# Kernel optimization log

Hardware: AMD Instinct MI355X
Metric: run time of the kernel (lower is better)

## Reference

```python
import jax, jax.numpy as jnp
import numpy as np
import math

B = 8192
N_MODELS = 64
T_PER_SPLIT = 16
MAXLEAF = 64
EMB = 32
BN_EPS = 1e-5


def setup_inputs() -> dict:
    key = jax.random.key(0)
    k1, k2, k3 = jax.random.split(key, 3)
    # leaf indices per (sample, model*tree), values in [0, maxleaf)
    x = jax.random.randint(k1, (B, N_MODELS * T_PER_SPLIT), 0, MAXLEAF, dtype=jnp.int32)
    # embed_w ~ N(0, sqrt(1/max_ntree_per_split))
    embed_w = jax.random.normal(k2, (N_MODELS, T_PER_SPLIT * MAXLEAF, EMB), dtype=jnp.float32) * math.sqrt(1.0 / T_PER_SPLIT)
    # BatchNorm1d affine params (gamma=1, beta=0 at init)
    bn_gamma = jnp.ones((N_MODELS * EMB,), dtype=jnp.float32)
    bn_beta = jnp.zeros((N_MODELS * EMB,), dtype=jnp.float32)
    # BatchDense(n_models, embsize, 1): weight (M, E, 1) squeezed to (M, E), bias zeros (M,)
    stdv = math.sqrt(6.0 / (EMB + 1))
    bout_w = jax.random.uniform(k3, (N_MODELS, EMB), dtype=jnp.float32, minval=-stdv, maxval=stdv)
    bout_b = jnp.zeros((N_MODELS,), dtype=jnp.float32)
    return {"x": x, "embed_w": embed_w, "bn_gamma": bn_gamma, "bn_beta": bn_beta,
            "bout_w": bout_w, "bout_b": bout_b}


def reference(x, embed_w, bn_gamma, bn_beta, bout_w, bout_b):
    # x: (B, M*T) int leaf indices; embed_w: (M, T*L, E)
    Bn = x.shape[0]
    M, TL, E = embed_w.shape
    T = x.shape[1] // M
    L = TL // T
    # one_hot + bmm == per-tree gather from embed_w, summed over trees
    idx = x.reshape(Bn, M, T) + jnp.arange(T, dtype=x.dtype) * L  # (B, M, T) into TL axis
    emb = embed_w[jnp.arange(M)[None, :, None], idx]              # (B, M, T, E) gather
    h = emb.sum(axis=2).reshape(Bn, M * E)                        # (B, M*E)
    # BatchNorm1d (training-mode batch statistics, biased variance as in torch)
    mean = h.mean(axis=0)
    var = h.var(axis=0)
    h = (h - mean) / jnp.sqrt(var + BN_EPS) * bn_gamma + bn_beta
    # dropout is identity in eval mode
    h = h.reshape(Bn, M, E)
    # BatchDense: per-model linear E -> 1
    out = jnp.einsum('bme,me->bm', h, bout_w) + bout_b            # (B, M)
    sum_out = out.sum(axis=-1, keepdims=True)                     # (B, 1)
    return (sum_out, out)
```

## Files before the change

### kernel.cpp

```cpp
#include <hip/hip_runtime.h>
#include <hip/hip_fp16.h>

constexpr int B_TOT = 8192;
constexpr int NM    = 64;
constexpr int TT    = 16;
constexpr int LF    = 64;
constexpr int EM    = 32;
constexpr int XROW  = NM * TT;
constexpr int TROWS = TT * LF;

__global__ __launch_bounds__(512, 4) void k_stats_f16(
    const int* __restrict__ x, const float* __restrict__ tbl,
    float* __restrict__ wsum, float* __restrict__ wsumsq)
{
    __shared__ uint4 tb[TROWS * 4];
    __shared__ float red[2][8][32];

    const int m     = blockIdx.x & 63;
    const int chunk = blockIdx.x >> 6;
    const int tid   = threadIdx.x;
    const int f     = tid & 3;
    const int grp   = tid >> 2;
    const int b0    = chunk * 1024;

    {
        const float4* __restrict__ src = (const float4*)(tbl + (size_t)m * (TROWS * EM));
#pragma unroll
        for (int i = 0; i < 8; ++i) {
            const int o = tid + i * 512;
            const float4 a = src[o * 2];
            const float4 c = src[o * 2 + 1];
            uint4 p;
            __half2 h0 = __floats2half2_rn(a.x, a.y);
            __half2 h1 = __floats2half2_rn(a.z, a.w);
            __half2 h2 = __floats2half2_rn(c.x, c.y);
            __half2 h3 = __floats2half2_rn(c.z, c.w);
            p.x = *(unsigned*)&h0; p.y = *(unsigned*)&h1;
            p.z = *(unsigned*)&h2; p.w = *(unsigned*)&h3;
            tb[o] = p;
        }
    }

    const int4* xp = (const int4*)(x + (size_t)(b0 + grp) * XROW + m * TT);
    int4 xa = xp[0], xb_ = xp[1], xc = xp[2], xd = xp[3];

    float s[8], s2[8];
#pragma unroll
    for (int k = 0; k < 8; ++k) { s[k] = 0.f; s2[k] = 0.f; }

    __syncthreads();

    for (int p = 0; p < 8; ++p) {
        int4 na, nb, nc, nd;
        if (p < 7) {
            const int4* np = (const int4*)(x + (size_t)(b0 + (p + 1) * 128 + grp) * XROW + m * TT);
            na = np[0]; nb = np[1]; nc = np[2]; nd = np[3];
        }

        __half2 h[4];
#pragma unroll
        for (int k = 0; k < 4; ++k) h[k] = __half2(__half(0.f), __half(0.f));

#pragma unroll
        for (int tq = 0; tq < 4; ++tq) {
            const int4 q = (tq == 0) ? xa : (tq == 1) ? xb_ : (tq == 2) ? xc : xd;
            const int rbase = tq * 256;
            const uint4 v0 = tb[(q.x + rbase      ) * 4 + f];
            const uint4 v1 = tb[(q.y + rbase +  64) * 4 + f];
            const uint4 v2 = tb[(q.z + rbase + 128) * 4 + f];
            const uint4 v3 = tb[(q.w + rbase + 192) * 4 + f];
            h[0] = __hadd2(h[0], __hadd2(__hadd2(*(const __half2*)&v0.x, *(const __half2*)&v1.x),
                                         __hadd2(*(const __half2*)&v2.x, *(const __half2*)&v3.x)));
            h[1] = __hadd2(h[1], __hadd2(__hadd2(*(const __half2*)&v0.y, *(const __half2*)&v1.y),
                                         __hadd2(*(const __half2*)&v2.y, *(const __half2*)&v3.y)));
            h[2] = __hadd2(h[2], __hadd2(__hadd2(*(const __half2*)&v0.z, *(const __half2*)&v1.z),
                                         __hadd2(*(const __half2*)&v2.z, *(const __half2*)&v3.z)));
            h[3] = __hadd2(h[3], __hadd2(__hadd2(*(const __half2*)&v0.w, *(const __half2*)&v1.w),
                                         __hadd2(*(const __half2*)&v2.w, *(const __half2*)&v3.w)));
        }

#pragma unroll
        for (int k = 0; k < 4; ++k) {
            const float lo = __low2float(h[k]);
            const float hi = __high2float(h[k]);
            s[2*k]   += lo;  s2[2*k]   = fmaf(lo, lo, s2[2*k]);
            s[2*k+1] += hi;  s2[2*k+1] = fmaf(hi, hi, s2[2*k+1]);
        }

        xa = na; xb_ = nb; xc = nc; xd = nd;
    }

#pragma unroll
    for (int off = 4; off <= 32; off <<= 1) {
#pragma unroll
        for (int k = 0; k < 8; ++k) {
            s[k]  += __shfl_xor(s[k],  off);
            s2[k] += __shfl_xor(s2[k], off);
        }
    }
    const int wave = tid >> 6;
    if ((tid & 63) < 4) {
#pragma unroll
        for (int k = 0; k < 8; ++k) {
            red[0][wave][f * 8 + k] = s[k];
            red[1][wave][f * 8 + k] = s2[k];
        }
    }
    __syncthreads();
    if (tid < 32) {
        float a = 0.f, a2 = 0.f;
#pragma unroll
        for (int w = 0; w < 8; ++w) { a += red[0][w][tid]; a2 += red[1][w][tid]; }
        atomicAdd(&wsum[m * EM + tid], a);
        atomicAdd(&wsumsq[m * EM + tid], a2);
    }
}

__global__ __launch_bounds__(256) void k_prep(
    const float* __restrict__ tbl,
    const float* __restrict__ gamma, const float* __restrict__ beta,
    const float* __restrict__ bw, const float* __restrict__ bb,
    const float* __restrict__ wsum, const float* __restrict__ wsumsq,
    float* __restrict__ Cm, float* __restrict__ g2)
{
    const int m    = blockIdx.x >> 2;
    const int part = blockIdx.x & 3;
    __shared__ float a_s[EM];
    if (threadIdx.x < EM) {
        const int e  = threadIdx.x;
        const int ch = m * EM + e;
        const float inv_n = 1.f / (float)B_TOT;
        const float mean = wsum[ch] * inv_n;
        const float var  = wsumsq[ch] * inv_n - mean * mean;
        const float istd = rsqrtf(var + 1e-5f);
        const float g = gamma[ch];
        const float w = bw[ch];
        a_s[e] = istd * g * w;
        float ct = (beta[ch] - mean * istd * g) * w;
#pragma unroll
        for (int off = 16; off > 0; off >>= 1) ct += __shfl_down(ct, off, 32);
        if (e == 0 && part == 0) Cm[m] = bb[m] + ct;
    }
    __syncthreads();

    const float* __restrict__ tblm = tbl + (size_t)m * (TROWS * EM);
    const int row = part * 256 + threadIdx.x;
    const float4* rp = (const float4*)(tblm + row * EM);
    float acc = 0.f;
#pragma unroll
    for (int i = 0; i < 8; ++i) {
        const float4 v = rp[i];
        acc += v.x * a_s[i*4+0] + v.y * a_s[i*4+1]
             + v.z * a_s[i*4+2] + v.w * a_s[i*4+3];
    }
    g2[row * NM + m] = acc;
}

__global__ __launch_bounds__(1024, 8) void k_out(
    const int* __restrict__ x, const float* __restrict__ g2,
    const float* __restrict__ Cm, float* __restrict__ out)
{
    __shared__ float slab[4 * LF * NM];
    const int tid  = threadIdx.x;
    const int wid  = tid >> 6;
    const int lane = tid & 63;
    const int b    = blockIdx.x * 16 + wid;

    const int4* xp = (const int4*)(x + (size_t)b * XROW + lane * TT);
    const int4 q0 = xp[0], q1 = xp[1], q2 = xp[2], q3 = xp[3];
    const int idxs[16] = {q0.x,q0.y,q0.z,q0.w, q1.x,q1.y,q1.z,q1.w,
                          q2.x,q2.y,q2.z,q2.w, q3.x,q3.y,q3.z,q3.w};

    float acc = 0.f;
#pragma unroll
    for (int ph = 0; ph < 4; ++ph) {
        if (ph) __syncthreads();
        const float4* src = (const float4*)(g2 + (size_t)ph * (4 * LF * NM));
        float4* dst = (float4*)slab;
#pragma unroll
        for (int j = 0; j < 4; ++j) dst[tid + j * 1024] = src[tid + j * 1024];
        __syncthreads();
#pragma unroll
        for (int tt = 0; tt < 4; ++tt)
            acc += slab[tt * (LF * NM) + idxs[ph * 4 + tt] * NM + lane];
    }

    const float o = acc + Cm[lane];
    float s = o;
#pragma unroll
    for (int off = 32; off > 0; off >>= 1) s += __shfl_down(s, off);
    out[B_TOT + (size_t)b * NM + lane] = o;
    if (lane == 0) out[b] = s;
}

extern "C" void kernel_launch(void* const* d_in, const int* in_sizes, int n_in,
                              void* d_out, int out_size, void* d_ws, size_t ws_size,
                              hipStream_t stream) {
    const int*   x       = (const int*)d_in[0];
    const float* embed_w = (const float*)d_in[1];
    const float* gamma   = (const float*)d_in[2];
    const float* beta    = (const float*)d_in[3];
    const float* bout_w  = (const float*)d_in[4];
    const float* bout_b  = (const float*)d_in[5];
    float* out = (float*)d_out;

    float* ws     = (float*)d_ws;
    float* wsum   = ws;
    float* wsumsq = ws + 2048;
    float* Cm     = ws + 4096;
    float* g2     = ws + 4160;

    (void)hipMemsetAsync(wsum, 0, 4096 * sizeof(float), stream);

    k_stats_f16<<<dim3(512), dim3(512), 0, stream>>>(x, embed_w, wsum, wsumsq);
    k_prep<<<dim3(256), dim3(256),  0, stream>>>(embed_w, gamma, beta, bout_w,
                                                 bout_b, wsum, wsumsq, Cm, g2);
    k_out <<<dim3(512), dim3(1024), 0, stream>>>(x, g2, Cm, out);
}
```

Measured before the change: 111.4 us.

## Load x rows cooperatively with DPP broadcast and drop memset via per-chunk partials

In the stats kernel, each of the four lanes sharing a sample now loads only one int4 of that sample's leaf indices instead of all four, and DPP quad broadcasts share the values across the quad. This cuts redundant global loads and register pressure. The atomic accumulation into zeroed buffers is replaced by per-chunk partial sums that k_prep adds up, which removes the memset launch and the atomics. The cost is four extra DPP moves per gathered int4 and eight partial reads per channel in k_prep.

Result: faster. 108.0 us (-3.0%).

```diff
diff --git a/kernel.cpp b/kernel.cpp
--- a/kernel.cpp
+++ b/kernel.cpp
@@ -9,9 +9,22 @@
 constexpr int XROW  = NM * TT;
 constexpr int TROWS = TT * LF;
 
+template<int TQ>
+__device__ __forceinline__ int4 qbcast(int4 v) {
+    constexpr int c = TQ * 0x55;
+    int4 r;
+    r.x = __builtin_amdgcn_mov_dpp(v.x, c, 0xf, 0xf, true);
+    r.y = __builtin_amdgcn_mov_dpp(v.y, c, 0xf, 0xf, true);
+    r.z = __builtin_amdgcn_mov_dpp(v.z, c, 0xf, 0xf, true);
+    r.w = __builtin_amdgcn_mov_dpp(v.w, c, 0xf, 0xf, true);
+    return r;
+}
+
+__device__ __forceinline__ __half2 H2(unsigned u) { return *(const __half2*)&u; }
+
 __global__ __launch_bounds__(512, 4) void k_stats_f16(
     const int* __restrict__ x, const float* __restrict__ tbl,
-    float* __restrict__ wsum, float* __restrict__ wsumsq)
+    float* __restrict__ psum, float* __restrict__ psq)
 {
     __shared__ uint4 tb[TROWS * 4];
     __shared__ float red[2][8][32];
@@ -41,8 +54,7 @@
         }
     }
 
-    const int4* xp = (const int4*)(x + (size_t)(b0 + grp) * XROW + m * TT);
-    int4 xa = xp[0], xb_ = xp[1], xc = xp[2], xd = xp[3];
+    int4 xr = ((const int4*)(x + (size_t)(b0 + grp) * XROW + m * TT))[f];
 
     float s[8], s2[8];
 #pragma unroll
@@ -51,43 +63,45 @@
     __syncthreads();
 
     for (int p = 0; p < 8; ++p) {
-        int4 na, nb, nc, nd;
-        if (p < 7) {
-            const int4* np = (const int4*)(x + (size_t)(b0 + (p + 1) * 128 + grp) * XROW + m * TT);
-            na = np[0]; nb = np[1]; nc = np[2]; nd = np[3];
-        }
-
-        __half2 h[4];
-#pragma unroll
-        for (int k = 0; k < 4; ++k) h[k] = __half2(__half(0.f), __half(0.f));
-
-#pragma unroll
-        for (int tq = 0; tq < 4; ++tq) {
-            const int4 q = (tq == 0) ? xa : (tq == 1) ? xb_ : (tq == 2) ? xc : xd;
-            const int rbase = tq * 256;
-            const uint4 v0 = tb[(q.x + rbase      ) * 4 + f];
-            const uint4 v1 = tb[(q.y + rbase +  64) * 4 + f];
-            const uint4 v2 = tb[(q.z + rbase + 128) * 4 + f];
-            const uint4 v3 = tb[(q.w + rbase + 192) * 4 + f];
-            h[0] = __hadd2(h[0], __hadd2(__hadd2(*(const __half2*)&v0.x, *(const __half2*)&v1.x),
-                                         __hadd2(*(const __half2*)&v2.x, *(const __half2*)&v3.x)));
-            h[1] = __hadd2(h[1], __hadd2(__hadd2(*(const __half2*)&v0.y, *(const __half2*)&v1.y),
-                                         __hadd2(*(const __half2*)&v2.y, *(const __half2*)&v3.y)));
-            h[2] = __hadd2(h[2], __hadd2(__hadd2(*(const __half2*)&v0.z, *(const __half2*)&v1.z),
-                                         __hadd2(*(const __half2*)&v2.z, *(const __half2*)&v3.z)));
-            h[3] = __hadd2(h[3], __hadd2(__hadd2(*(const __half2*)&v0.w, *(const __half2*)&v1.w),
-                                         __hadd2(*(const __half2*)&v2.w, *(const __half2*)&v3.w)));
-        }
-
+        int4 nxt;
+        if (p < 7)
+            nxt = ((const int4*)(x + (size_t)(b0 + (p + 1) * 128 + grp) * XROW + m * TT))[f];
+
+        const int4 q0 = qbcast<0>(xr);
+        const int4 q1 = qbcast<1>(xr);
+        const int4 q2 = qbcast<2>(xr);
+        const int4 q3 = qbcast<3>(xr);
+
+        __half2 h0 = __half2(__half(0.f), __half(0.f));
+        __half2 h1 = h0, h2 = h0, h3 = h0;
+
+#define GATH(Q, RB)                                                          \
+        {                                                                    \
+            const uint4 a0 = tb[((Q).x + RB      ) * 4 + f];                 \
+            const uint4 a1 = tb[((Q).y + RB +  64) * 4 + f];                 \
+            const uint4 a2 = tb[((Q).z + RB + 128) * 4 + f];                 \
+            const uint4 a3 = tb[((Q).w + RB + 192) * 4 + f];                 \
+            h0 = __hadd2(h0, __hadd2(__hadd2(H2(a0.x), H2(a1.x)),            \
+                                     __hadd2(H2(a2.x), H2(a3.x))));          \
+            h1 = __hadd2(h1, __hadd2(__hadd2(H2(a0.y), H2(a1.y)),            \
+                                     __hadd2(H2(a2.y), H2(a3.y))));          \
+            h2 = __hadd2(h2, __hadd2(__hadd2(H2(a0.z), H2(a1.z)),            \
+                                     __hadd2(H2(a2.z), H2(a3.z))));          \
+            h3 = __hadd2(h3, __hadd2(__hadd2(H2(a0.w), H2(a1.w)),            \
+                                     __hadd2(H2(a2.w), H2(a3.w))));          \
+        }
+        GATH(q0, 0) GATH(q1, 256) GATH(q2, 512) GATH(q3, 768)
+#undef GATH
+
+        const __half2 hv[4] = {h0, h1, h2, h3};
 #pragma unroll
         for (int k = 0; k < 4; ++k) {
-            const float lo = __low2float(h[k]);
-            const float hi = __high2float(h[k]);
+            const float lo = __low2float(hv[k]);
+            const float hi = __high2float(hv[k]);
             s[2*k]   += lo;  s2[2*k]   = fmaf(lo, lo, s2[2*k]);
             s[2*k+1] += hi;  s2[2*k+1] = fmaf(hi, hi, s2[2*k+1]);
         }
-
-        xa = na; xb_ = nb; xc = nc; xd = nd;
+        xr = nxt;
     }
 
 #pragma unroll
@@ -111,8 +125,8 @@
         float a = 0.f, a2 = 0.f;
 #pragma unroll
         for (int w = 0; w < 8; ++w) { a += red[0][w][tid]; a2 += red[1][w][tid]; }
-        atomicAdd(&wsum[m * EM + tid], a);
-        atomicAdd(&wsumsq[m * EM + tid], a2);
+        psum[(chunk * NM + m) * EM + tid] = a;
+        psq [(chunk * NM + m) * EM + tid] = a2;
     }
 }
 
@@ -120,7 +134,7 @@
     const float* __restrict__ tbl,
     const float* __restrict__ gamma, const float* __restrict__ beta,
     const float* __restrict__ bw, const float* __restrict__ bb,
-    const float* __restrict__ wsum, const float* __restrict__ wsumsq,
+    const float* __restrict__ psum, const float* __restrict__ psq,
     float* __restrict__ Cm, float* __restrict__ g2)
 {
     const int m    = blockIdx.x >> 2;
@@ -129,9 +143,15 @@
     if (threadIdx.x < EM) {
         const int e  = threadIdx.x;
         const int ch = m * EM + e;
+        float sum = 0.f, sq = 0.f;
+#pragma unroll
+        for (int c = 0; c < 8; ++c) {
+            sum += psum[(c * NM + m) * EM + e];
+            sq  += psq [(c * NM + m) * EM + e];
+        }
         const float inv_n = 1.f / (float)B_TOT;
-        const float mean = wsum[ch] * inv_n;
-        const float var  = wsumsq[ch] * inv_n - mean * mean;
+        const float mean = sum * inv_n;
+        const float var  = sq * inv_n - mean * mean;
         const float istd = rsqrtf(var + 1e-5f);
         const float g = gamma[ch];
         const float w = bw[ch];
@@ -204,16 +224,14 @@
     const float* bout_b  = (const float*)d_in[5];
     float* out = (float*)d_out;
 
-    float* ws     = (float*)d_ws;
-    float* wsum   = ws;
-    float* wsumsq = ws + 2048;
-    float* Cm     = ws + 4096;
-    float* g2     = ws + 4160;
-
-    (void)hipMemsetAsync(wsum, 0, 4096 * sizeof(float), stream);
-
-    k_stats_f16<<<dim3(512), dim3(512), 0, stream>>>(x, embed_w, wsum, wsumsq);
+    float* ws   = (float*)d_ws;
+    float* Cm   = ws;
+    float* g2   = ws + 64;
+    float* psum = ws + 64 + 65536;
+    float* psq  = psum + 16384;
+
+    k_stats_f16<<<dim3(512), dim3(512), 0, stream>>>(x, embed_w, psum, psq);
     k_prep<<<dim3(256), dim3(256),  0, stream>>>(embed_w, gamma, beta, bout_w,
-                                                 bout_b, wsum, wsumsq, Cm, g2);
+                                                 bout_b, psum, psq, Cm, g2);
     k_out <<<dim3(512), dim3(1024), 0, stream>>>(x, g2, Cm, out);
 }
```
